# Performance work log

Hardware: AMD Instinct MI355X
Metric: run time of the kernel (lower is better)

The kernel has to match this reference:

```python
import jax, jax.numpy as jnp
import numpy as np

B, N, C, H = 64, 197, 768, 12
CH = C // H            # 64 head dim
RC = CH // 2           # 32 reduced channel
RN = N // 8            # 24 reduced tokens
TOPK_COEF = 8
BUDGET = int(np.ceil(0.25 * N))   # 50
BASIS_THRESH = 0.02
MP_SCALE = H ** -0.5               # MaskPredictor: num_heads**-0.5 (as in source)
ATTN_SCALE = CH ** -0.5
LN_EPS = 1e-5


def _ln(x, g, b):
    mu = x.mean(-1, keepdims=True)
    var = ((x - mu) ** 2).mean(-1, keepdims=True)
    return (x - mu) * jax.lax.rsqrt(var + LN_EPS) * g + b


def _keep_topk(x, k):
    # zero all but the k largest along last axis (tie-break by value threshold)
    kth = jax.lax.top_k(x, k)[0][..., -1:]
    return jnp.where(x >= kth, x, 0.0)


def setup_inputs() -> dict:
    key = jax.random.key(0)
    ks = jax.random.split(key, 20)
    d = {}
    d['x'] = jax.random.normal(ks[0], (B, N, C), jnp.float32)
    s = 0.02
    d['Wqkv'] = jax.random.normal(ks[1], (C, 3 * C), jnp.float32) * s
    d['Wcq'] = jax.random.normal(ks[2], (CH, RC), jnp.float32) * s
    d['bcq'] = jnp.zeros((RC,), jnp.float32)
    d['Wck'] = jax.random.normal(ks[3], (CH, RC), jnp.float32) * s
    d['bck'] = jnp.zeros((RC,), jnp.float32)
    d['proj_n'] = jax.random.normal(ks[4], (N, RN), jnp.float32) * s
    d['proj_back_n'] = jax.random.normal(ks[5], (N, RN), jnp.float32) * s
    d['Wproj'] = jax.random.normal(ks[6], (C, C), jnp.float32) * s
    d['bproj'] = jnp.zeros((C,), jnp.float32)
    d['g1'] = jnp.ones((C,), jnp.float32)
    d['b1'] = jnp.zeros((C,), jnp.float32)
    d['g2'] = jnp.ones((C,), jnp.float32)
    d['b2'] = jnp.zeros((C,), jnp.float32)
    d['W1'] = jax.random.normal(ks[7], (C, 4 * C), jnp.float32) * s
    d['bfc1'] = jnp.zeros((4 * C,), jnp.float32)
    d['W2'] = jax.random.normal(ks[8], (4 * C, C), jnp.float32) * s
    d['bfc2'] = jnp.zeros((C,), jnp.float32)
    return d


def reference(x, Wqkv, Wcq, bcq, Wck, bck, proj_n, proj_back_n, Wproj, bproj,
              g1, b1, g2, b2, W1, bfc1, W2, bfc2):
    h = _ln(x, g1, b1)
    qkv = (h @ Wqkv).reshape(B, N, 3, H, CH).transpose(2, 0, 3, 1, 4)  # [3,B,H,N,CH]
    q, k, v = qkv[0], qkv[1], qkv[2]

    # ---- MaskPredictor (eval path) ----
    qp = q @ Wcq + bcq                                # [B,H,N,RC]
    kp = k @ Wck + bck                                # [B,H,N,RC]
    kk = jnp.einsum('bhnc,nr->bhcr', kp, proj_n)      # [B,H,RC,RN]
    cheap = jnp.einsum('bhnc,bhcr->bhnr', qp, kk) * MP_SCALE
    cheap = cheap[:, :, 1:, :]                        # drop cls query row
    basis_coef = jax.nn.softmax(cheap, axis=-1)       # [B,H,N-1,RN]
    basis_coef = _keep_topk(basis_coef, TOPK_COEF)
    basis = jnp.abs(proj_back_n.T)                    # [RN,N]
    basis = jnp.where(basis > BASIS_THRESH, basis, 0.0)
    approx_attn = basis_coef @ basis                  # [B,H,N-1,N]
    kth = jax.lax.top_k(approx_attn, BUDGET)[0][..., -1:]
    mask = approx_attn >= kth                         # [B,H,N-1,N] bool
    cls_mask = jnp.ones((B, H, 1, N), bool)
    attn_mask = jnp.concatenate([cls_mask, mask], axis=2)  # [B,H,N,N]

    # ---- masked full attention ----
    attn = jnp.einsum('bhqc,bhkc->bhqk', q * ATTN_SCALE, k)
    attn = jnp.where(attn_mask, attn, -jnp.inf)
    attn = jax.nn.softmax(attn, axis=-1)
    out = jnp.einsum('bhqk,bhkc->bhqc', attn, v)
    out = out.transpose(0, 2, 1, 3).reshape(B, N, C)
    out = out @ Wproj + bproj

    x = x + out                                       # skip_lam = 1.0
    h2 = _ln(x, g2, b2)
    mlp = jax.nn.gelu(h2 @ W1 + bfc1, approximate=False) @ W2 + bfc2
    x = x + mlp
    return x
```

## Files before the change

kernel.cpp:

```cpp
#include <hip/hip_runtime.h>
#include <math.h>
#include <float.h>

#define B_ 64
#define N_ 197
#define C_ 768
#define H_ 12
#define CH_ 64
#define RC_ 32
#define RN_ 24

typedef __attribute__((ext_vector_type(8))) short short8;
typedef __attribute__((ext_vector_type(4))) float f32x4;
typedef __attribute__((address_space(3))) void  lds_void;
typedef __attribute__((address_space(1))) const void g_void;

__device__ __forceinline__ float warp_sum(float v){
  #pragma unroll
  for(int o=32;o>=1;o>>=1) v += __shfl_xor(v,o);
  return v;
}
__device__ __forceinline__ float warp_max(float v){
  #pragma unroll
  for(int o=32;o>=1;o>>=1) v = fmaxf(v,__shfl_xor(v,o));
  return v;
}
__device__ __forceinline__ unsigned short f2bf(float f){
  union{float f; unsigned u;} c; c.f = f;
  unsigned r = c.u + 0x7FFF + ((c.u>>16)&1);
  return (unsigned short)(r>>16);
}
__device__ __forceinline__ float bf2f(unsigned short u){
  union{unsigned u; float f;} c; c.u = ((unsigned)u)<<16; return c.f;
}
__device__ __forceinline__ int2 xcd_swz(int gx, int gy){
  int nwg = gx*gy;
  int id = blockIdx.x + gx*blockIdx.y;
  int xcd = id & 7, loc = id >> 3;
  int q = nwg >> 3, r = nwg & 7;
  int swz = (xcd < r ? xcd*(q+1) : r*(q+1) + (xcd-r)*q) + loc;
  return make_int2(swz % gx, swz / gx);
}

__global__ __launch_bounds__(256) void ln_kernel(const float* __restrict__ x,
    const float* __restrict__ g, const float* __restrict__ bb, unsigned short* __restrict__ out){
  int r = blockIdx.x; int tid = threadIdx.x;
  const float* xr = x + (size_t)r*C_;
  float v0=xr[tid], v1=xr[tid+256], v2=xr[tid+512];
  __shared__ float red[8];
  float s = warp_sum(v0+v1+v2);
  if((tid&63)==0) red[tid>>6]=s;
  __syncthreads();
  float mu = (red[0]+red[1]+red[2]+red[3]) * (1.f/768.f);
  float d0=v0-mu,d1=v1-mu,d2=v2-mu;
  float s2 = warp_sum(d0*d0+d1*d1+d2*d2);
  if((tid&63)==0) red[4+(tid>>6)]=s2;
  __syncthreads();
  float rinv = rsqrtf((red[4]+red[5]+red[6]+red[7])*(1.f/768.f)+1e-5f);
  unsigned short* orow = out + (size_t)r*C_;
  orow[tid]     = f2bf(d0*rinv*g[tid]    +bb[tid]);
  orow[tid+256] = f2bf(d1*rinv*g[tid+256]+bb[tid+256]);
  orow[tid+512] = f2bf(d2*rinv*g[tid+512]+bb[tid+512]);
}

__global__ __launch_bounds__(256) void wtrans_kernel(const float* __restrict__ in,
    unsigned short* __restrict__ out, int K, int N){
  __shared__ float tile[32][33];
  int n0 = blockIdx.x*32, k0 = blockIdx.y*32;
  int tx = threadIdx.x&31, ty = threadIdx.x>>5;
  #pragma unroll
  for(int i=0;i<4;++i) tile[ty+8*i][tx] = in[(size_t)(k0+ty+8*i)*N + n0+tx];
  __syncthreads();
  #pragma unroll
  for(int i=0;i<4;++i) out[(size_t)(n0+ty+8*i)*K + k0+tx] = f2bf(tile[tx][ty+8*i]);
}

__global__ __launch_bounds__(256) void wcprep_kernel(const float* __restrict__ Wcq,
    const float* __restrict__ Wck, unsigned short* __restrict__ WcqT,
    unsigned short* __restrict__ WckT){
  int t = blockIdx.x*256 + threadIdx.x;
  if(t < 2048){
    int c = t>>6, k = t&63;
    WcqT[t] = f2bf(Wcq[k*32+c]);
    WckT[t] = f2bf(Wck[k*32+c]);
  }
}

template<int ACT, int RESID, int OUTBF16>
__global__ __launch_bounds__(256) void gemm_bf16(
    const unsigned short* __restrict__ A, const unsigned short* __restrict__ WT,
    const float* __restrict__ bias, const float* __restrict__ resid,
    void* __restrict__ Cout, int M, int K, int Nc){
  __shared__ unsigned short As[2*128*32];
  __shared__ unsigned short Bs[2*128*32];
  int tid = threadIdx.x, lane = tid&63, wid = tid>>6;
  int2 bxy = xcd_swz(gridDim.x, gridDim.y);
  int m0 = bxy.y*128, n0 = bxy.x*128;
  int wr = wid>>1, wc = wid&1;
  int lm = lane&15, lg = lane>>4;
  int lgs = lg ^ ((lm>>1)&3);
  int row0 = tid>>2,         kc0 = (((tid&3) ^ ((tid>>3)&3)))*8;
  int row1 = (256+tid)>>2,   kc1 = kc0;
  int ar0 = m0+row0; if(ar0 > M-1) ar0 = M-1;
  int ar1 = m0+row1; if(ar1 > M-1) ar1 = M-1;
  const unsigned short* gA0 = A  + (size_t)ar0*K + kc0;
  const unsigned short* gA1 = A  + (size_t)ar1*K + kc1;
  const unsigned short* gB0 = WT + (size_t)(n0+row0)*K + kc0;
  const unsigned short* gB1 = WT + (size_t)(n0+row1)*K + kc1;
  unsigned short* lA0 = As + (wid*64)*8;
  unsigned short* lA1 = As + (256 + wid*64)*8;
  unsigned short* lB0 = Bs + (wid*64)*8;
  unsigned short* lB1 = Bs + (256 + wid*64)*8;

#define STAGE_(buf, kt) do{ \
    __builtin_amdgcn_global_load_lds((g_void*)(gA0 + (kt)), (lds_void*)(lA0 + (buf)*4096), 16, 0, 0); \
    __builtin_amdgcn_global_load_lds((g_void*)(gB0 + (kt)), (lds_void*)(lB0 + (buf)*4096), 16, 0, 0); \
    __builtin_amdgcn_global_load_lds((g_void*)(gA1 + (kt)), (lds_void*)(lA1 + (buf)*4096), 16, 0, 0); \
    __builtin_amdgcn_global_load_lds((g_void*)(gB1 + (kt)), (lds_void*)(lB1 + (buf)*4096), 16, 0, 0); \
  }while(0)

  f32x4 acc[4][4] = {};
  const int nt = K/32;
  STAGE_(0, 0);
  __syncthreads();
  for(int t=0; t<nt; t+=2){
    STAGE_(1, (t+1)*32);
    {
      short8 af[4], bfv[4];
      #pragma unroll
      for(int i=0;i<4;++i){
        af[i]  = *(const short8*)(As + (64*wr + 16*i + lm)*32 + lgs*8);
        bfv[i] = *(const short8*)(Bs + (64*wc + 16*i + lm)*32 + lgs*8);
      }
      #pragma unroll
      for(int i=0;i<4;++i)
        #pragma unroll
        for(int j=0;j<4;++j)
          acc[i][j] = __builtin_amdgcn_mfma_f32_16x16x32_bf16(af[i], bfv[j], acc[i][j], 0,0,0);
    }
    __syncthreads();
    if(t+2 < nt) STAGE_(0, (t+2)*32);
    {
      short8 af[4], bfv[4];
      #pragma unroll
      for(int i=0;i<4;++i){
        af[i]  = *(const short8*)(As + 4096 + (64*wr + 16*i + lm)*32 + lgs*8);
        bfv[i] = *(const short8*)(Bs + 4096 + (64*wc + 16*i + lm)*32 + lgs*8);
      }
      #pragma unroll
      for(int i=0;i<4;++i)
        #pragma unroll
        for(int j=0;j<4;++j)
          acc[i][j] = __builtin_amdgcn_mfma_f32_16x16x32_bf16(af[i], bfv[j], acc[i][j], 0,0,0);
    }
    __syncthreads();
  }
#undef STAGE_
  #pragma unroll
  for(int i=0;i<4;++i){
    #pragma unroll
    for(int j=0;j<4;++j){
      int gcol = n0 + 64*wc + 16*j + lm;
      float bv = bias ? bias[gcol] : 0.f;
      #pragma unroll
      for(int r=0;r<4;++r){
        int grow = m0 + 64*wr + 16*i + lg*4 + r;
        if(grow < M){
          float cv = acc[i][j][r] + bv;
          if(ACT==1){
            float xx = cv;
            float p = xx*fmaf(xx*xx, 0.10294517f, 2.3022079f);
            float q = exp2f(p);
            cv = xx - xx*__builtin_amdgcn_rcpf(1.0f+q);
          }
          if(RESID) cv += resid[(size_t)grow*Nc + gcol];
          if(OUTBF16) ((unsigned short*)Cout)[(size_t)grow*Nc+gcol] = f2bf(cv);
          else        ((float*)Cout)[(size_t)grow*Nc+gcol] = cv;
        }
      }
    }
  }
}

template<int ACT, int RESID, int OUTBF16>
__global__ __launch_bounds__(512, 4) void gemm256_bf16(
    const unsigned short* __restrict__ A, const unsigned short* __restrict__ WT,
    const float* __restrict__ bias, const float* __restrict__ resid,
    void* __restrict__ Cout, int M, int K, int Nc){
  __shared__ unsigned short As[2*256*32];
  __shared__ unsigned short Bs[2*128*32];
  int tid = threadIdx.x, lane = tid&63, wid = tid>>6;
  int2 bxy = xcd_swz(gridDim.x, gridDim.y);
  int m0 = bxy.y*256, n0 = bxy.x*128;
  int wm = wid>>1, wn = wid&1;
  int lm = lane&15, lg = lane>>4;
  int lgs = lg ^ ((lm>>1)&3);
  int rowA0 = tid>>2, rowA1 = 128 + (tid>>2), rowB = tid>>2;
  int kc = (((tid&3) ^ ((tid>>3)&3)))*8;
  int arA0 = m0+rowA0; if(arA0 > M-1) arA0 = M-1;
  int arA1 = m0+rowA1; if(arA1 > M-1) arA1 = M-1;
  const unsigned short* gA0 = A  + (size_t)arA0*K + kc;
  const unsigned short* gA1 = A  + (size_t)arA1*K + kc;
  const unsigned short* gB0 = WT + (size_t)(n0+rowB)*K + kc;
  unsigned short* lA0 = As + wid*512;
  unsigned short* lA1 = As + 4096 + wid*512;
  unsigned short* lB0 = Bs + wid*512;

#define STAGE2_(buf, kt) do{ \
    __builtin_amdgcn_global_load_lds((g_void*)(gA0 + (kt)), (lds_void*)(lA0 + (buf)*8192), 16, 0, 0); \
    __builtin_amdgcn_global_load_lds((g_void*)(gB0 + (kt)), (lds_void*)(lB0 + (buf)*4096), 16, 0, 0); \
    __builtin_amdgcn_global_load_lds((g_void*)(gA1 + (kt)), (lds_void*)(lA1 + (buf)*8192), 16, 0, 0); \
  }while(0)

  f32x4 acc[4][4] = {};
  const int nt = K/32;
  STAGE2_(0, 0);
  __syncthreads();
  for(int t=0; t<nt; ++t){
    int buf = t&1;
    if(t+1 < nt) STAGE2_(buf^1, (t+1)*32);
    const unsigned short* abase = As + buf*8192;
    const unsigned short* bbase = Bs + buf*4096;
    short8 af[4], bfv[4];
    #pragma unroll
    for(int i=0;i<4;++i)
      af[i] = *(const short8*)(abase + (wm*64 + i*16 + lm)*32 + lgs*8);
    #pragma unroll
    for(int j=0;j<4;++j)
      bfv[j] = *(const short8*)(bbase + (wn*64 + j*16 + lm)*32 + lgs*8);
    __builtin_amdgcn_s_setprio(1);
    #pragma unroll
    for(int i=0;i<4;++i)
      #pragma unroll
      for(int j=0;j<4;++j)
        acc[i][j] = __builtin_amdgcn_mfma_f32_16x16x32_bf16(af[i], bfv[j], acc[i][j], 0,0,0);
    __builtin_amdgcn_s_setprio(0);
    __syncthreads();
  }
#undef STAGE2_
  #pragma unroll
  for(int i=0;i<4;++i){
    #pragma unroll
    for(int j=0;j<4;++j){
      int gcol = n0 + wn*64 + j*16 + lm;
      float bv = bias ? bias[gcol] : 0.f;
      #pragma unroll
      for(int r=0;r<4;++r){
        int grow = m0 + wm*64 + i*16 + lg*4 + r;
        if(grow < M){
          float cv = acc[i][j][r] + bv;
          if(ACT==1){
            float xx = cv;
            float p = xx*fmaf(xx*xx, 0.10294517f, 2.3022079f);
            float q = exp2f(p);
            cv = xx - xx*__builtin_amdgcn_rcpf(1.0f+q);
          }
          if(RESID) cv += resid[(size_t)grow*Nc + gcol];
          if(OUTBF16) ((unsigned short*)Cout)[(size_t)grow*Nc+gcol] = f2bf(cv);
          else        ((float*)Cout)[(size_t)grow*Nc+gcol] = cv;
        }
      }
    }
  }
}

__global__ __launch_bounds__(512) void cheap_kernel(
    const unsigned short* __restrict__ qkv,
    const unsigned short* __restrict__ WcqT, const float* __restrict__ bcq,
    const unsigned short* __restrict__ WckT, const float* __restrict__ bck,
    const float* __restrict__ proj_n, float* __restrict__ coef){
  int bh = blockIdx.x; int b = bh/H_, h = bh%H_;
  int tid = threadIdx.x, lane = tid&63, wv = tid>>6;
  int lm = lane&15, lg = lane>>4;
  __shared__ __align__(16) unsigned short KQ[208*64];
  __shared__ __align__(16) float P2T[32*212];
  __shared__ __align__(16) float PNT[24*200];
  __shared__ float KK[768];
  const unsigned short* Kbase = qkv + ((size_t)(b*N_)*3 + 1)*C_ + h*CH_;
  const unsigned short* Qbase = qkv + ((size_t)(b*N_)*3 + 0)*C_ + h*CH_;
  for(int idx = tid; idx < 208*32; idx += 512){
    int k = idx>>5, cp = idx&31;
    unsigned v = (k < N_) ? *(const unsigned*)(Kbase + (size_t)k*3*C_ + cp*2) : 0u;
    unsigned off = (unsigned)(k*128 + cp*4) ^ ((unsigned)(k&7)<<4);
    *(unsigned*)((char*)KQ + off) = v;
  }
  for(int idx = tid; idx < 24*200; idx += 512){
    int r = idx/200, n = idx - r*200;
    PNT[idx] = (n < N_) ? proj_n[n*24+r] : 0.f;
  }
  __syncthreads();
  {
    short8 bfr[2][2];
    #pragma unroll
    for(int j=0;j<2;++j)
      #pragma unroll
      for(int s=0;s<2;++s)
        bfr[j][s] = *(const short8*)(WckT + (j*16+lm)*64 + s*32 + lg*8);
    float bias[2] = { bck[lm], bck[16+lm] };
    for(int t=wv; t<13; t+=8){
      int row = t*16 + lm;
      unsigned o0 = (unsigned)(row*128 + lg*16) ^ ((unsigned)(row&7)<<4);
      unsigned o1 = (unsigned)(row*128 + 64 + lg*16) ^ ((unsigned)(row&7)<<4);
      short8 a0 = *(const short8*)((char*)KQ + o0);
      short8 a1 = *(const short8*)((char*)KQ + o1);
      #pragma unroll
      for(int j=0;j<2;++j){
        f32x4 acc = (f32x4){0.f,0.f,0.f,0.f};
        acc = __builtin_amdgcn_mfma_f32_16x16x32_bf16(a0, bfr[j][0], acc, 0,0,0);
        acc = __builtin_amdgcn_mfma_f32_16x16x32_bf16(a1, bfr[j][1], acc, 0,0,0);
        #pragma unroll
        for(int r=0;r<4;++r)
          P2T[(j*16+lm)*212 + t*16 + lg*4 + r] = acc[r] + bias[j];
      }
    }
  }
  __syncthreads();
  {
    int i0 = tid, i1 = tid + 512;
    bool has1 = (i1 < 768);
    int c0 = i0/24, r0 = i0 - c0*24;
    int c1 = has1 ? i1/24 : 0, r1 = has1 ? (i1 - (i1/24)*24) : 0;
    float a0=0.f, a1=0.f;
    for(int n=0;n<200;n+=4){
      float4 x0 = *(const float4*)&P2T[c0*212+n];
      float4 p0 = *(const float4*)&PNT[r0*200+n];
      a0 += x0.x*p0.x; a0 += x0.y*p0.y; a0 += x0.z*p0.z; a0 += x0.w*p0.w;
      if(has1){
        float4 x1 = *(const float4*)&P2T[c1*212+n];
        float4 p1 = *(const float4*)&PNT[r1*200+n];
        a1 += x1.x*p1.x; a1 += x1.y*p1.y; a1 += x1.z*p1.z; a1 += x1.w*p1.w;
      }
    }
    KK[i0] = a0;
    if(has1) KK[i1] = a1;
    for(int idx = tid; idx < 197*32; idx += 512){
      int k = idx>>5, cp = idx&31;
      unsigned v = *(const unsigned*)(Qbase + (size_t)k*3*C_ + cp*2);
      unsigned off = (unsigned)(k*128 + cp*4) ^ ((unsigned)(k&7)<<4);
      *(unsigned*)((char*)KQ + off) = v;
    }
  }
  __syncthreads();
  float* QP = P2T;
  {
    short8 bfr[2][2];
    #pragma unroll
    for(int j=0;j<2;++j)
      #pragma unroll
      for(int s=0;s<2;++s)
        bfr[j][s] = *(const short8*)(WcqT + (j*16+lm)*64 + s*32 + lg*8);
    float bias[2] = { bcq[lm], bcq[16+lm] };
    for(int t=wv; t<13; t+=8){
      int row = t*16 + lm;
      unsigned o0 = (unsigned)(row*128 + lg*16) ^ ((unsigned)(row&7)<<4);
      unsigned o1 = (unsigned)(row*128 + 64 + lg*16) ^ ((unsigned)(row&7)<<4);
      short8 a0 = *(const short8*)((char*)KQ + o0);
      short8 a1 = *(const short8*)((char*)KQ + o1);
      #pragma unroll
      for(int j=0;j<2;++j){
        f32x4 acc = (f32x4){0.f,0.f,0.f,0.f};
        acc = __builtin_amdgcn_mfma_f32_16x16x32_bf16(a0, bfr[j][0], acc, 0,0,0);
        acc = __builtin_amdgcn_mfma_f32_16x16x32_bf16(a1, bfr[j][1], acc, 0,0,0);
        #pragma unroll
        for(int r=0;r<4;++r)
          QP[(t*16 + lg*4 + r)*32 + j*16 + lm] = acc[r] + bias[j];
      }
    }
  }
  __syncthreads();
  int l32 = lane & 31, half = lane >> 5;
  bool act = l32 < RN_;
  int ll = act ? l32 : 0;
  float kkreg[32];
  #pragma unroll
  for(int c=0;c<32;++c) kkreg[c] = KK[c*24 + ll];
  for(int i2 = wv*2; i2 < 196; i2 += 16){
    int i = i2 + half;
    int n = i + 1;
    float accv = 0.f;
    #pragma unroll
    for(int q=0;q<8;++q){
      float4 v4 = *(const float4*)&QP[n*32 + q*4];
      accv += v4.x*kkreg[q*4];   accv += v4.y*kkreg[q*4+1];
      accv += v4.z*kkreg[q*4+2]; accv += v4.w*kkreg[q*4+3];
    }
    float val = act ? accv * 0.28867513459481287f : -INFINITY;
    float m = val;
    #pragma unroll
    for(int o=16;o>=1;o>>=1) m = fmaxf(m, __shfl_xor(m, o));
    float e = act ? expf(val - m) : 0.f;
    float ssum = e;
    #pragma unroll
    for(int o=16;o>=1;o>>=1) ssum += __shfl_xor(ssum, o);
    float p = e/ssum;
    unsigned u = __float_as_uint(e);
    unsigned pL=0, pH=0;
    #pragma unroll
    for(int bit=30; bit>=0; --bit){
      unsigned tL = pL | (1u<<bit), tH = pH | (1u<<bit);
      unsigned thr = half ? tH : tL;
      unsigned long long bal = __ballot(u >= thr);
      int cL = __popcll(bal & 0xFFFFFFull);
      int cH = __popcll((bal>>32) & 0xFFFFFFull);
      if(cL>=8) pL=tL;
      if(cH>=8) pH=tH;
    }
    unsigned myp = half ? pH : pL;
    if(act) coef[((size_t)bh*196 + i)*24 + l32] = (u >= myp) ? p : 0.f;
  }
}

__global__ __launch_bounds__(256) void basis_kernel(const float* __restrict__ pb,
    float* __restrict__ basis){
  int t = blockIdx.x*256 + threadIdx.x;
  if(t < RN_*N_){
    int r = t/N_, j = t%N_;
    float v = fabsf(pb[(size_t)j*RN_ + r]);
    basis[t] = (v > 0.02f) ? v : 0.f;
  }
}

__global__ __launch_bounds__(256) void mask8_kernel(const float* __restrict__ coef,
    const float* __restrict__ basis, unsigned int* __restrict__ maskw){
  __shared__ float Bs[24*256];
  int tid = threadIdx.x, lane = tid&63, wv = tid>>6;
  for(int idx = tid; idx < 24*256; idx += 256){
    int r = idx>>8, q = idx&255;
    int e = ((q&3)<<6) | (q>>2);
    Bs[idx] = (e < N_) ? basis[r*N_ + e] : 0.f;
  }
  __syncthreads();
  int rowbase = blockIdx.x*32 + wv*8;
  float4 av[8];
  unsigned done = 0;
  #pragma unroll
  for(int j=0;j<8;++j){
    int row = rowbase + j;
    int qi = row % N_; int bh = row / N_;
    if(qi==0){
      if(lane<8){
        unsigned v = (lane<6)?0xFFFFFFFFu:((lane==6)?0x1Fu:0u);
        maskw[(size_t)row*8+lane]=v;
      }
      av[j] = make_float4(0.f,0.f,0.f,0.f);
      done |= (1u<<j);
    } else {
      float cfv = (lane<24) ? coef[((size_t)bh*196 + (qi-1))*24 + lane] : 0.f;
      unsigned long long nz = __ballot(cfv != 0.f);
      float4 a = make_float4(0.f,0.f,0.f,0.f);
      while(nz){
        int r = __ffsll((unsigned long long)nz) - 1;
        nz &= nz - 1;
        float c = __uint_as_float(__builtin_amdgcn_readlane(__float_as_uint(cfv), r));
        float4 bv = *(const float4*)&Bs[r*256 + lane*4];
        a.x += c*bv.x; a.y += c*bv.y; a.z += c*bv.z; a.w += c*bv.w;
      }
      av[j] = a;
    }
  }
  unsigned u[8][4];
  #pragma unroll
  for(int j=0;j<8;++j){
    u[j][0]=__float_as_uint(av[j].x); u[j][1]=__float_as_uint(av[j].y);
    u[j][2]=__float_as_uint(av[j].z); u[j][3]=__float_as_uint(av[j].w);
  }
  unsigned prefix[8] = {0,0,0,0,0,0,0,0};
  for(int bit=30; bit>=0; --bit){
    if(done == 0xFFu) break;
    #pragma unroll
    for(int j=0;j<8;++j){
      if((done>>j)&1u) continue;
      unsigned t = prefix[j] | (1u<<bit);
      int c = __popcll(__ballot(u[j][0] >= t)) + __popcll(__ballot(u[j][1] >= t))
            + __popcll(__ballot(u[j][2] >= t)) + __popcll(__ballot(u[j][3] >= t));
      if(c >= 50) prefix[j] = t;
      if(c == 50) done |= (1u<<j);
    }
  }
  #pragma unroll
  for(int j=0;j<8;++j){
    int row = rowbase + j;
    if(row % N_ == 0) continue;
    #pragma unroll
    for(int r=0;r<4;++r){
      bool valid = (r<3) | (lane<5);
      bool keep = valid && (u[j][r] >= prefix[j]);
      unsigned long long bal = __ballot(keep);
      if(lane==0){
        maskw[(size_t)row*8 + 2*r]   = (unsigned)(bal & 0xFFFFFFFFull);
        maskw[(size_t)row*8 + 2*r+1] = (unsigned)(bal>>32);
      }
    }
  }
}

__global__ __launch_bounds__(512) void attn3_kernel(const unsigned short* __restrict__ qkv,
    const unsigned int* __restrict__ maskw, unsigned short* __restrict__ attn_out){
  int bh = blockIdx.x; int b = bh/H_, h = bh%H_;
  int tid = threadIdx.x, lane = tid&63, wv = tid>>6;
  int g = lane>>4, c16 = lane&15;
  __shared__ unsigned short Kb[208*64];
  __shared__ unsigned short Vt[64*220];
  __shared__ unsigned short Pl[8*16*224];
  __shared__ unsigned int   Ml[8][16][8];
  const unsigned short* Kbase = qkv + ((size_t)(b*N_)*3 + 1)*C_ + h*CH_;
  const unsigned short* Vbase = qkv + ((size_t)(b*N_)*3 + 2)*C_ + h*CH_;
  for(int idx = tid; idx < 208*32; idx += 512){
    int k = idx>>5, cp = idx&31;
    unsigned pk = 0;
    if(k < N_) pk = *(const unsigned*)(Kbase + (size_t)k*3*C_ + cp*2);
    unsigned off = (unsigned)(k*128 + cp*4) ^ ((unsigned)(k&7)<<4);
    *(unsigned*)((char*)Kb + off) = pk;
  }
  for(int idx = tid; idx < 64*110; idx += 512){
    int kp = idx>>6, c = idx&63;
    int k0 = kp*2, k1 = kp*2+1;
    unsigned v0 = (k0<N_) ? Vbase[(size_t)k0*3*C_ + c] : 0;
    unsigned v1 = (k1<N_) ? Vbase[(size_t)k1*3*C_ + c] : 0;
    *(unsigned*)((char*)Vt + c*440 + kp*4) = v0 | (v1<<16);
  }
  __syncthreads();
  size_t pbase = (size_t)wv*16*448;
  for(int i=lane;i<128;i+=64){
    int ql = i>>3; int kk = 208 + (i&7)*2;
    unsigned off = (unsigned)(ql*448 + kk*2) ^ ((unsigned)(ql&7)<<4);
    *(unsigned*)((char*)Pl + pbase + off) = 0u;
  }
  for(int t = wv; t < 13; t += 8){
    int qb = t*16;
    for(int i = lane; i < 128; i += 64){
      int row = i>>3, word = i&7;
      int qr = qb+row; if(qr>196) qr=196;
      Ml[wv][row][word] = maskw[(size_t)(bh*N_+qr)*8 + word];
    }
    int qrow = qb + c16; if(qrow>196) qrow=196;
    const unsigned short* Qr = qkv + ((size_t)(b*N_+qrow)*3)*C_ + h*CH_ + g*8;
    short8 af[2];
    af[0] = *(const short8*)(Qr);
    af[1] = *(const short8*)(Qr + 32);
    f32x4 sf[13];
    #pragma unroll
    for(int f=0;f<13;++f){
      sf[f] = (f32x4){0.f,0.f,0.f,0.f};
      #pragma unroll
      for(int s=0;s<2;++s){
        int row = f*16 + c16;
        unsigned off = (unsigned)(row*128 + s*64 + g*16) ^ ((unsigned)(row&7)<<4);
        short8 bfr = *(const short8*)((char*)Kb + off);
        sf[f] = __builtin_amdgcn_mfma_f32_16x16x32_bf16(af[s], bfr, sf[f], 0,0,0);
      }
      sf[f][0]*=0.125f; sf[f][1]*=0.125f; sf[f][2]*=0.125f; sf[f][3]*=0.125f;
    }
    unsigned keep[4] = {0,0,0,0};
    float m[4] = {-FLT_MAX,-FLT_MAX,-FLT_MAX,-FLT_MAX};
    #pragma unroll
    for(int f=0;f<13;++f)
      #pragma unroll
      for(int r=0;r<4;++r){
        unsigned bit = (Ml[wv][g*4+r][f>>1] >> ((f&1)*16 + c16)) & 1u;
        keep[r] |= bit<<f;
        if(bit) m[r] = fmaxf(m[r], sf[f][r]);
      }
    #pragma unroll
    for(int r=0;r<4;++r){
      #pragma unroll
      for(int o=8;o>=1;o>>=1) m[r] = fmaxf(m[r], __shfl_xor(m[r], o));
    }
    float sum[4] = {0,0,0,0};
    #pragma unroll
    for(int f=0;f<13;++f)
      #pragma unroll
      for(int r=0;r<4;++r){
        float e = ((keep[r]>>f)&1u) ? expf(sf[f][r]-m[r]) : 0.f;
        sf[f][r] = e; sum[r] += e;
      }
    #pragma unroll
    for(int r=0;r<4;++r){
      #pragma unroll
      for(int o=8;o>=1;o>>=1) sum[r] += __shfl_xor(sum[r], o);
      sum[r] = 1.f/sum[r];
    }
    #pragma unroll
    for(int f=0;f<13;++f)
      #pragma unroll
      for(int r=0;r<4;++r){
        int ql = g*4+r;
        unsigned off = (unsigned)(ql*448 + (f*16+c16)*2) ^ ((unsigned)(ql&7)<<4);
        *(unsigned short*)((char*)Pl + pbase + off) = f2bf(sf[f][r]*sum[r]);
      }
    #pragma unroll
    for(int ct=0;ct<4;++ct){
      f32x4 oa = (f32x4){0.f,0.f,0.f,0.f};
      #pragma unroll
      for(int ks=0;ks<7;++ks){
        unsigned offa = (unsigned)(c16*448 + (ks*32+g*8)*2) ^ ((unsigned)(c16&7)<<4);
        short8 pa = *(const short8*)((char*)Pl + pbase + offa);
        short8 vb = *(const short8*)((char*)Vt + (size_t)(ct*16+c16)*440 + (ks*32+g*8)*2);
        oa = __builtin_amdgcn_mfma_f32_16x16x32_bf16(pa, vb, oa, 0,0,0);
      }
      #pragma unroll
      for(int r=0;r<4;++r){
        int qq = qb + g*4 + r;
        if(qq < N_)
          attn_out[((size_t)(b*N_+qq))*C_ + h*CH_ + ct*16 + c16] = f2bf(oa[r]);
      }
    }
  }
}

extern "C" void kernel_launch(void* const* d_in, const int* in_sizes, int n_in,
                              void* d_out, int out_size, void* d_ws, size_t ws_size,
                              hipStream_t stream){
  const float* x    =(const float*)d_in[0];
  const float* Wqkv =(const float*)d_in[1];
  const float* Wcq  =(const float*)d_in[2];
  const float* bcq  =(const float*)d_in[3];
  const float* Wck  =(const float*)d_in[4];
  const float* bck  =(const float*)d_in[5];
  const float* proj_n=(const float*)d_in[6];
  const float* proj_back_n=(const float*)d_in[7];
  const float* Wproj=(const float*)d_in[8];
  const float* bproj=(const float*)d_in[9];
  const float* g1=(const float*)d_in[10];
  const float* b1=(const float*)d_in[11];
  const float* g2=(const float*)d_in[12];
  const float* b2=(const float*)d_in[13];
  const float* W1=(const float*)d_in[14];
  const float* bfc1=(const float*)d_in[15];
  const float* W2=(const float*)d_in[16];
  const float* bfc2=(const float*)d_in[17];
  float* out=(float*)d_out;

  float* ws=(float*)d_ws;
  size_t off=0;
  unsigned short* hbuf = (unsigned short*)(ws+off); off += (size_t)12608*768/2;
  size_t qkv_off = off;
  unsigned short* qkv = (unsigned short*)(ws+off); off += (size_t)12608*2304/2;
  off += (size_t)768*197*32;
  off += (size_t)768*197*32;
  off += (size_t)768*32*24;
  float* coef = ws+off;        off += (size_t)768*196*24;
  float* basis= ws+off;        off += 4736;
  unsigned int* maskw=(unsigned int*)(ws+off); off += (size_t)768*197*8;
  unsigned short* WqkvT = (unsigned short*)(ws+off); off += (size_t)2304*768/2;
  unsigned short* WprojT= (unsigned short*)(ws+off); off += (size_t)768*768/2;
  unsigned short* W1T   = (unsigned short*)(ws+off); off += (size_t)3072*768/2;
  unsigned short* W2T   = (unsigned short*)(ws+off); off += (size_t)768*3072/2;
  unsigned short* WcqT  = (unsigned short*)(ws+off); off += 1024;
  unsigned short* WckT  = (unsigned short*)(ws+off); off += 1024;
  unsigned short* attn_out = hbuf;
  unsigned short* hidden = (unsigned short*)(ws+qkv_off);
  float* x1 = out;

  wtrans_kernel<<<dim3(72,24),256,0,stream>>>(Wqkv, WqkvT, 768, 2304);
  wtrans_kernel<<<dim3(24,24),256,0,stream>>>(Wproj, WprojT, 768, 768);
  wtrans_kernel<<<dim3(96,24),256,0,stream>>>(W1, W1T, 768, 3072);
  wtrans_kernel<<<dim3(24,96),256,0,stream>>>(W2, W2T, 3072, 768);
  wcprep_kernel<<<8,256,0,stream>>>(Wcq, Wck, WcqT, WckT);
  ln_kernel<<<12608,256,0,stream>>>(x,g1,b1,hbuf);
  gemm256_bf16<0,0,1><<<dim3(18,50),512,0,stream>>>(hbuf,WqkvT,nullptr,nullptr,qkv,12608,768,2304);
  cheap_kernel<<<768,512,0,stream>>>(qkv,WcqT,bcq,WckT,bck,proj_n,coef);
  basis_kernel<<<19,256,0,stream>>>(proj_back_n,basis);
  mask8_kernel<<<4728,256,0,stream>>>(coef,basis,maskw);
  attn3_kernel<<<768,512,0,stream>>>(qkv,maskw,attn_out);
  gemm_bf16<0,1,0><<<dim3(6,99),256,0,stream>>>(attn_out,WprojT,bproj,x,x1,12608,768,768);
  ln_kernel<<<12608,256,0,stream>>>(x1,g2,b2,hbuf);
  gemm256_bf16<1,0,1><<<dim3(24,50),512,0,stream>>>(hbuf,W1T,bfc1,nullptr,hidden,12608,768,3072);
  gemm_bf16<0,1,0><<<dim3(6,99),256,0,stream>>>(hidden,W2T,bfc2,x1,out,12608,3072,768);
}
```

Measured before the change: 642.3 us.

## Use 64x128 tiles for N=768 GEMMs to fill more CUs

Replaces the 128x128-tile GEMM used for the output projection and the second MLP layer with a 64x128-tile variant. This raises the grid from 594 to 1182 blocks, so the 256 CUs see better wave balance. Each wave now owns a 64x32 output slice. The K loop switches to a single-stage double-buffer with one barrier per step and raises wave priority around the MFMA block. The trade-off is lower arithmetic intensity per tile, more redundant reads of B, and more barriers per unit of work.

```diff
diff --git a/kernel.cpp b/kernel.cpp
--- a/kernel.cpp
+++ b/kernel.cpp
@@ -87,84 +87,69 @@
 }
 
 template<int ACT, int RESID, int OUTBF16>
-__global__ __launch_bounds__(256) void gemm_bf16(
+__global__ __launch_bounds__(256) void gemm64_bf16(
     const unsigned short* __restrict__ A, const unsigned short* __restrict__ WT,
     const float* __restrict__ bias, const float* __restrict__ resid,
     void* __restrict__ Cout, int M, int K, int Nc){
-  __shared__ unsigned short As[2*128*32];
+  __shared__ unsigned short As[2*64*32];
   __shared__ unsigned short Bs[2*128*32];
   int tid = threadIdx.x, lane = tid&63, wid = tid>>6;
   int2 bxy = xcd_swz(gridDim.x, gridDim.y);
-  int m0 = bxy.y*128, n0 = bxy.x*128;
-  int wr = wid>>1, wc = wid&1;
+  int m0 = bxy.y*64, n0 = bxy.x*128;
+  int wc = wid;
   int lm = lane&15, lg = lane>>4;
   int lgs = lg ^ ((lm>>1)&3);
-  int row0 = tid>>2,         kc0 = (((tid&3) ^ ((tid>>3)&3)))*8;
-  int row1 = (256+tid)>>2,   kc1 = kc0;
-  int ar0 = m0+row0; if(ar0 > M-1) ar0 = M-1;
-  int ar1 = m0+row1; if(ar1 > M-1) ar1 = M-1;
-  const unsigned short* gA0 = A  + (size_t)ar0*K + kc0;
-  const unsigned short* gA1 = A  + (size_t)ar1*K + kc1;
-  const unsigned short* gB0 = WT + (size_t)(n0+row0)*K + kc0;
-  const unsigned short* gB1 = WT + (size_t)(n0+row1)*K + kc1;
-  unsigned short* lA0 = As + (wid*64)*8;
-  unsigned short* lA1 = As + (256 + wid*64)*8;
-  unsigned short* lB0 = Bs + (wid*64)*8;
-  unsigned short* lB1 = Bs + (256 + wid*64)*8;
-
-#define STAGE_(buf, kt) do{ \
-    __builtin_amdgcn_global_load_lds((g_void*)(gA0 + (kt)), (lds_void*)(lA0 + (buf)*4096), 16, 0, 0); \
+  int rowA = tid>>2;
+  int kc   = (((tid&3) ^ ((tid>>3)&3)))*8;
+  int arA = m0+rowA; if(arA > M-1) arA = M-1;
+  const unsigned short* gA0 = A  + (size_t)arA*K + kc;
+  const unsigned short* gB0 = WT + (size_t)(n0 + (tid>>2))*K + kc;
+  const unsigned short* gB1 = WT + (size_t)(n0 + 64 + (tid>>2))*K + kc;
+  unsigned short* lA0 = As + wid*512;
+  unsigned short* lB0 = Bs + wid*512;
+  unsigned short* lB1 = Bs + 2048 + wid*512;
+
+#define STAGE64_(buf, kt) do{ \
+    __builtin_amdgcn_global_load_lds((g_void*)(gA0 + (kt)), (lds_void*)(lA0 + (buf)*2048), 16, 0, 0); \
     __builtin_amdgcn_global_load_lds((g_void*)(gB0 + (kt)), (lds_void*)(lB0 + (buf)*4096), 16, 0, 0); \
-    __builtin_amdgcn_global_load_lds((g_void*)(gA1 + (kt)), (lds_void*)(lA1 + (buf)*4096), 16, 0, 0); \
     __builtin_amdgcn_global_load_lds((g_void*)(gB1 + (kt)), (lds_void*)(lB1 + (buf)*4096), 16, 0, 0); \
   }while(0)
 
-  f32x4 acc[4][4] = {};
+  f32x4 acc[4][2] = {};
   const int nt = K/32;
-  STAGE_(0, 0);
-  __syncthreads();
-  for(int t=0; t<nt; t+=2){
-    STAGE_(1, (t+1)*32);
-    {
-      short8 af[4], bfv[4];
-      #pragma unroll
-      for(int i=0;i<4;++i){
-        af[i]  = *(const short8*)(As + (64*wr + 16*i + lm)*32 + lgs*8);
-        bfv[i] = *(const short8*)(Bs + (64*wc + 16*i + lm)*32 + lgs*8);
-      }
-      #pragma unroll
-      for(int i=0;i<4;++i)
-        #pragma unroll
-        for(int j=0;j<4;++j)
-          acc[i][j] = __builtin_amdgcn_mfma_f32_16x16x32_bf16(af[i], bfv[j], acc[i][j], 0,0,0);
-    }
+  STAGE64_(0, 0);
+  __syncthreads();
+  for(int t=0; t<nt; ++t){
+    int buf = t&1;
+    if(t+1 < nt) STAGE64_(buf^1, (t+1)*32);
+    const unsigned short* abase = As + buf*2048;
+    const unsigned short* bbase = Bs + buf*4096;
+    short8 af[4], bfv[2];
+    #pragma unroll
+    for(int i=0;i<4;++i)
+      af[i] = *(const short8*)(abase + (16*i + lm)*32 + lgs*8);
+    #pragma unroll
+    for(int j=0;j<2;++j)
+      bfv[j] = *(const short8*)(bbase + (wc*32 + 16*j + lm)*32 + lgs*8);
+    __builtin_amdgcn_s_setprio(1);
+    #pragma unroll
+    for(int i=0;i<4;++i)
+      #pragma unroll
+      for(int j=0;j<2;++j)
+        acc[i][j] = __builtin_amdgcn_mfma_f32_16x16x32_bf16(af[i], bfv[j], acc[i][j], 0,0,0);
+    __builtin_amdgcn_s_setprio(0);
     __syncthreads();
-    if(t+2 < nt) STAGE_(0, (t+2)*32);
-    {
-      short8 af[4], bfv[4];
-      #pragma unroll
-      for(int i=0;i<4;++i){
-        af[i]  = *(const short8*)(As + 4096 + (64*wr + 16*i + lm)*32 + lgs*8);
-        bfv[i] = *(const short8*)(Bs + 4096 + (64*wc + 16*i + lm)*32 + lgs*8);
-      }
-      #pragma unroll
-      for(int i=0;i<4;++i)
-        #pragma unroll
-        for(int j=0;j<4;++j)
-          acc[i][j] = __builtin_amdgcn_mfma_f32_16x16x32_bf16(af[i], bfv[j], acc[i][j], 0,0,0);
-    }
-    __syncthreads();
-  }
-#undef STAGE_
+  }
+#undef STAGE64_
   #pragma unroll
   for(int i=0;i<4;++i){
     #pragma unroll
-    for(int j=0;j<4;++j){
-      int gcol = n0 + 64*wc + 16*j + lm;
+    for(int j=0;j<2;++j){
+      int gcol = n0 + wc*32 + 16*j + lm;
       float bv = bias ? bias[gcol] : 0.f;
       #pragma unroll
       for(int r=0;r<4;++r){
-        int grow = m0 + 64*wr + 16*i + lg*4 + r;
+        int grow = m0 + 16*i + lg*4 + r;
         if(grow < M){
           float cv = acc[i][j][r] + bv;
           if(ACT==1){
@@ -663,8 +648,8 @@
   basis_kernel<<<19,256,0,stream>>>(proj_back_n,basis);
   mask8_kernel<<<4728,256,0,stream>>>(coef,basis,maskw);
   attn3_kernel<<<768,512,0,stream>>>(qkv,maskw,attn_out);
-  gemm_bf16<0,1,0><<<dim3(6,99),256,0,stream>>>(attn_out,WprojT,bproj,x,x1,12608,768,768);
+  gemm64_bf16<0,1,0><<<dim3(6,197),256,0,stream>>>(attn_out,WprojT,bproj,x,x1,12608,768,768);
   ln_kernel<<<12608,256,0,stream>>>(x1,g2,b2,hbuf);
   gemm256_bf16<1,0,1><<<dim3(24,50),512,0,stream>>>(hbuf,W1T,bfc1,nullptr,hidden,12608,768,3072);
-  gemm_bf16<0,1,0><<<dim3(6,99),256,0,stream>>>(hidden,W2T,bfc2,x1,out,12608,3072,768);
-}
+  gemm64_bf16<0,1,0><<<dim3(6,197),256,0,stream>>>(hidden,W2T,bfc2,x1,out,12608,3072,768);
+}
```

Result: no change. 642.2 us (-0.0%).
